# Kernel tuning notes

Hardware: AMD Instinct MI355X
Metric: run time of the kernel (lower is better)

Reference implementation:

```python
import jax, jax.numpy as jnp
import numpy as np

N = 100000   # n_node
D = 64       # emb_size
NNZ = 3200000
B, L = 64, 200
LAYERS = 2


def setup_inputs() -> dict:
    key = jax.random.key(0)
    ks = jax.random.split(key, 12)
    s = 1.0 / np.sqrt(D)  # reset_parameters uniform(-stdv, stdv)
    u = lambda k, shape: jax.random.uniform(k, shape, minval=-s, maxval=s, dtype=jnp.float32)
    return {
        "input": jax.random.randint(ks[0], (B, L), 0, N).astype(jnp.int32),
        "h_item_idx": jax.random.randint(ks[1], (2, NNZ), 0, N).astype(jnp.int32),
        "h_item_val": jax.random.uniform(ks[2], (NNZ,), dtype=jnp.float32),
        "h_user_idx": jax.random.randint(ks[3], (2, NNZ), 0, N).astype(jnp.int32),
        "h_user_val": jax.random.uniform(ks[4], (NNZ,), dtype=jnp.float32),
        "user_emb": u(ks[5], (N, D)),
        "w0": u(ks[6], (D, D)),
        "w1": u(ks[7], (D, D)),
        "b0": u(ks[8], (1, D)),
        "b1": u(ks[9], (1, D)),
        "att": u(ks[10], (1, D)),
        "att_m": u(ks[11], (D, D)),
    }


def _spmm(idx, val, x):
    # torch.sparse.mm(H, x) with H given as COO (rows=idx[0], cols=idx[1])
    gathered = val[:, None] * x[idx[1]]              # [nnz, D]
    return jax.ops.segment_sum(gathered, idx[0], num_segments=N)


def _l2norm(x):
    # F.normalize(x, p=2, dim=1), eps=1e-12
    n = jnp.maximum(jnp.linalg.norm(x, axis=1, keepdims=True), 1e-12)
    return x / n


def _structure_embed(h_item_idx, h_item_val, h_user_idx, h_user_val,
                     user_emb, w0, w1, b0, b1, att, att_m):
    # self_gating per channel (eval mode: no graph dropout)
    e2 = user_emb * jax.nn.sigmoid(user_emb @ w0 + b0)
    e3 = user_emb * jax.nn.sigmoid(user_emb @ w1 + b1)
    acc2, acc3 = e2, e3
    for _ in range(LAYERS):
        e2 = _spmm(h_item_idx, h_item_val, e2)
        acc2 = acc2 + _l2norm(e2)
        e3 = _spmm(h_user_idx, h_user_val, e3)
        acc3 = acc3 + _l2norm(e3)
    # channel attention over the two channel embeddings
    w_c2 = jnp.sum(att * (acc2 @ att_m), axis=1)     # [N]
    w_c3 = jnp.sum(att * (acc3 @ att_m), axis=1)     # [N]
    score = jax.nn.softmax(jnp.stack([w_c2, w_c3], axis=1), axis=-1)  # [N, 2]
    mixed = score[:, 0:1] * acc2 + score[:, 1:2] * acc3
    return mixed


def reference(input, h_item_idx, h_item_val, h_user_idx, h_user_val,
              user_emb, w0, w1, b0, b1, att, att_m):
    mask = input == 0                                 # [B, L]
    hg = _structure_embed(h_item_idx, h_item_val, h_user_idx, h_user_val,
                          user_emb, w0, w1, b0, b1, att, att_m)
    cas_seq_emb = hg[input]                           # [B, L, D]
    source_emb = cas_seq_emb[:, 0, :]                 # [B, D]
    # long-term attention: source query attends over the cascade sequence
    scores = jnp.einsum("bd,bld->bl", source_emb, cas_seq_emb) / np.sqrt(D)
    scores = jnp.where(mask, -1e9, scores)
    attw = jax.nn.softmax(scores, axis=-1)            # [B, L]
    L_cas_emb = attw[:, :, None] * cas_seq_emb        # [B, L, D]
    return (L_cas_emb, cas_seq_emb)
```

## Files before the change

### kernel.cpp

```cpp
#include <hip/hip_runtime.h>
#include <cstdint>
#include <cstddef>

#define N_NODES 100000
#define D 64
#define NNZ 3200000
#define BB 64
#define LL 200
#define BSHIFT 7
#define BSIZE 128
#define NBUCK 782
#define CAP 4608
#define EPT 9
#define BM_WORDS 3200

__device__ __forceinline__ float wave_sum(float x) {
#pragma unroll
  for (int o = 32; o; o >>= 1) x += __shfl_xor(x, o, 64);
  return x;
}

__global__ void mark_kernel(const int* __restrict__ input, uint32_t* __restrict__ bm,
                            int* __restrict__ list, int* __restrict__ nlist) {
  int t = blockIdx.x * 256 + threadIdx.x;
  if (t < BB * LL) {
    int i = input[t];
    uint32_t bit = 1u << (i & 31);
    uint32_t old = atomicOr(&bm[i >> 5], bit);
    if (!(old & bit)) {
      int p = atomicAdd(nlist, 1);
      list[p] = i;
    }
  }
}

__global__ __launch_bounds__(256) void gate_kernel(
    const float* __restrict__ u, const float* __restrict__ w0,
    const float* __restrict__ w1, const float* __restrict__ b0,
    const float* __restrict__ b1, float* __restrict__ e2, float* __restrict__ e3) {
  __shared__ float sw0[D * D];
  __shared__ float sw1[D * D];
  __shared__ float sb0[D], sb1[D];
  for (int t = threadIdx.x; t < D * D; t += 256) { sw0[t] = w0[t]; sw1[t] = w1[t]; }
  if (threadIdx.x < D) { sb0[threadIdx.x] = b0[threadIdx.x]; sb1[threadIdx.x] = b1[threadIdx.x]; }
  __syncthreads();
  int wave = (blockIdx.x * 256 + threadIdx.x) >> 6;
  int lane = threadIdx.x & 63;
  int nw = (gridDim.x * 256) >> 6;
  for (int i = wave; i < N_NODES; i += nw) {
    float uv = u[i * D + lane];
    float a0 = 0.f, a1 = 0.f;
#pragma unroll
    for (int k = 0; k < D; ++k) {
      float uk = __shfl(uv, k, 64);
      a0 = fmaf(uk, sw0[k * D + lane], a0);
      a1 = fmaf(uk, sw1[k * D + lane], a1);
    }
    a0 += sb0[lane];
    a1 += sb1[lane];
    float s0 = 1.f / (1.f + expf(-a0));
    float s1 = 1.f / (1.f + expf(-a1));
    e2[i * D + lane] = uv * s0;
    e3[i * D + lane] = uv * s1;
  }
}

__global__ void init_cursor_kernel(uint32_t* __restrict__ gcursor) {
  int t = blockIdx.x * 256 + threadIdx.x;
  if (t < NBUCK) gcursor[t] = (uint32_t)t * CAP;
}

__global__ __launch_bounds__(1024) void bin_kernel(
    const int* __restrict__ dsts, const int* __restrict__ srcs,
    const float* __restrict__ val, uint32_t* __restrict__ gcursor,
    uint2* __restrict__ binned) {
  __shared__ uint32_t hist[NBUCK];
  __shared__ uint32_t gbase[NBUCK];
  const int CHUNK = 8192;
  int base = blockIdx.x * CHUNK;
  int tid = threadIdx.x;
  for (int t = tid; t < NBUCK; t += 1024) hist[t] = 0u;
  __syncthreads();
  int n = NNZ - base;
  if (n > CHUNK) n = CHUNK;
  uint32_t px[8]; float pv[8]; uint32_t pb[8]; uint32_t pr[8];
#pragma unroll
  for (int k = 0; k < 8; ++k) {
    int off = (k << 10) + tid;
    bool ok = off < n;
    int e = base + off;
    int d = ok ? dsts[e] : 0;
    int s = ok ? srcs[e] : 0;
    float v = ok ? val[e] : 0.f;
    uint32_t b = (uint32_t)d >> BSHIFT;
    pb[k] = ok ? b : 0xFFFFFFFFu;
    pr[k] = ok ? atomicAdd(&hist[b], 1u) : 0u;
    px[k] = (uint32_t)s | ((uint32_t)(d & (BSIZE - 1)) << 17);
    pv[k] = v;
  }
  __syncthreads();
  for (int t = tid; t < NBUCK; t += 1024) {
    uint32_t h = hist[t];
    gbase[t] = h ? atomicAdd(&gcursor[t], h) : 0u;
  }
  __syncthreads();
#pragma unroll
  for (int k = 0; k < 8; ++k) {
    if (pb[k] != 0xFFFFFFFFu) {
      uint32_t pos = gbase[pb[k]] + pr[k];
      uint32_t lim = (pb[k] + 1u) * CAP;
      if (pos < lim) {
        binned[pos] = make_uint2(px[k], __float_as_uint(pv[k]));
      }
    }
  }
}

__global__ __launch_bounds__(512) void sortspmm_kernel(
    const uint32_t* __restrict__ gcursor, uint2* __restrict__ binned,
    const float* __restrict__ xin, float* __restrict__ xout,
    uint32_t* __restrict__ grow_start, uint32_t* __restrict__ grow_cnt) {
  __shared__ uint2 sp[CAP];
  __shared__ uint32_t hist[BSIZE];
  __shared__ uint32_t ssc[BSIZE];
  __shared__ uint32_t sst[BSIZE];
  int bucket = blockIdx.x, tid = threadIdx.x;
  int nodebase = bucket << BSHIFT;
  uint32_t cnt = gcursor[bucket] - (uint32_t)bucket * CAP;
  if (cnt > CAP) cnt = CAP;
  if (tid < BSIZE) hist[tid] = 0u;
  __syncthreads();
  uint2 pr[EPT]; uint32_t rk[EPT];
  const uint2* ep = binned + (size_t)bucket * CAP;
#pragma unroll
  for (int k = 0; k < EPT; ++k) {
    int e = (k << 9) + tid;
    if (e < (int)cnt) {
      pr[k] = ep[e];
      rk[k] = atomicAdd(&hist[pr[k].x >> 17], 1u);
    }
  }
  __syncthreads();
  if (tid < BSIZE) ssc[tid] = hist[tid];
  __syncthreads();
  for (int o = 1; o < BSIZE; o <<= 1) {
    uint32_t t = 0;
    if (tid < BSIZE && tid >= o) t = ssc[tid - o];
    __syncthreads();
    if (tid < BSIZE) ssc[tid] += t;
    __syncthreads();
  }
  if (tid < BSIZE) sst[tid] = ssc[tid] - hist[tid];
  __syncthreads();
#pragma unroll
  for (int k = 0; k < EPT; ++k) {
    int e = (k << 9) + tid;
    if (e < (int)cnt) sp[sst[pr[k].x >> 17] + rk[k]] = pr[k];
  }
  __syncthreads();
  for (int t = tid; t < (int)cnt; t += 512) binned[(size_t)bucket * CAP + t] = sp[t];
  int nvalid = N_NODES - nodebase;
  if (nvalid > BSIZE) nvalid = BSIZE;
  if (tid < nvalid) {
    grow_start[nodebase + tid] = (uint32_t)bucket * CAP + sst[tid];
    grow_cnt[nodebase + tid] = hist[tid];
  }
  int wave = tid >> 6, lane = tid & 63, g = lane >> 4, c = lane & 15;
  for (int r = wave; r < nvalid; r += 8) {
    uint32_t rc = hist[r], s0 = sst[r];
    float ax = 0.f, ay = 0.f, az = 0.f, aw = 0.f;
    uint32_t rc4 = (rc + 3u) & ~3u;
    for (uint32_t j = 0; j < rc4; j += 4) {
      uint32_t e = j + (uint32_t)g;
      uint2 p = make_uint2(0u, 0u);
      if (e < rc) p = sp[s0 + e];
      float v = __uint_as_float(p.y);
      uint32_t src = p.x & 0x1FFFFu;
      float4 xv = ((const float4*)(xin + (size_t)src * D))[c];
      ax = fmaf(v, xv.x, ax); ay = fmaf(v, xv.y, ay);
      az = fmaf(v, xv.z, az); aw = fmaf(v, xv.w, aw);
    }
#pragma unroll
    for (int o = 16; o <= 32; o <<= 1) {
      ax += __shfl_xor(ax, o, 64); ay += __shfl_xor(ay, o, 64);
      az += __shfl_xor(az, o, 64); aw += __shfl_xor(aw, o, 64);
    }
    if (g == 0)
      ((float4*)(xout + (size_t)(nodebase + r) * D))[c] = make_float4(ax, ay, az, aw);
  }
}

__global__ __launch_bounds__(256) void listspmm_kernel(
    const uint32_t* __restrict__ grow_start, const uint32_t* __restrict__ grow_cnt,
    const uint2* __restrict__ pairs, const float* __restrict__ xin,
    float* __restrict__ xout, const int* __restrict__ list, const int* __restrict__ nlist) {
  int wave = (blockIdx.x * 256 + threadIdx.x) >> 6;
  int lane = threadIdx.x & 63;
  int nw = (gridDim.x * 256) >> 6;
  int g = lane >> 4, c = lane & 15;
  int n = nlist[0];
  for (int ii = wave; ii < n; ii += nw) {
    int i = list[ii];
    uint32_t rc = grow_cnt[i];
    uint32_t base = grow_start[i];
    float ax = 0.f, ay = 0.f, az = 0.f, aw = 0.f;
    uint32_t rc4 = (rc + 3u) & ~3u;
    for (uint32_t j = 0; j < rc4; j += 4) {
      uint32_t e = j + (uint32_t)g;
      uint2 p = make_uint2(0u, 0u);
      if (e < rc) p = pairs[base + e];
      float v = __uint_as_float(p.y);
      uint32_t src = p.x & 0x1FFFFu;
      float4 xv = ((const float4*)(xin + (size_t)src * D))[c];
      ax = fmaf(v, xv.x, ax); ay = fmaf(v, xv.y, ay);
      az = fmaf(v, xv.z, az); aw = fmaf(v, xv.w, aw);
    }
#pragma unroll
    for (int o = 16; o <= 32; o <<= 1) {
      ax += __shfl_xor(ax, o, 64); ay += __shfl_xor(ay, o, 64);
      az += __shfl_xor(az, o, 64); aw += __shfl_xor(aw, o, 64);
    }
    if (g == 0)
      ((float4*)(xout + (size_t)i * D))[c] = make_float4(ax, ay, az, aw);
  }
}

__global__ __launch_bounds__(256) void final_kernel(
    const int* __restrict__ input,
    const float* __restrict__ e20, const float* __restrict__ e21, const float* __restrict__ e22,
    const float* __restrict__ e30, const float* __restrict__ e31, const float* __restrict__ e32,
    const float* __restrict__ att, const float* __restrict__ att_m,
    float* __restrict__ out_Lcas, float* __restrict__ out_cas) {
  __shared__ float cas[LL * D];
  __shared__ float sv[D];
  __shared__ float sscore[LL];
  __shared__ float red[8];
  int b = blockIdx.x, tid = threadIdx.x;
  if (tid < D) {
    float a = 0.f;
#pragma unroll
    for (int j = 0; j < D; ++j) a = fmaf(att_m[tid * D + j], att[j], a);
    sv[tid] = a;
  }
  __syncthreads();
  int wv = tid >> 6, lane = tid & 63;
  float svl = sv[lane];
  for (int l = wv; l < LL; l += 4) {
    int i = input[b * LL + l];
    size_t o = (size_t)i * D + lane;
    float v20 = e20[o], v21 = e21[o], v22 = e22[o];
    float v30 = e30[o], v31 = e31[o], v32 = e32[o];
    float n21 = fmaxf(sqrtf(wave_sum(v21 * v21)), 1e-12f);
    float n22 = fmaxf(sqrtf(wave_sum(v22 * v22)), 1e-12f);
    float n31 = fmaxf(sqrtf(wave_sum(v31 * v31)), 1e-12f);
    float n32 = fmaxf(sqrtf(wave_sum(v32 * v32)), 1e-12f);
    float a2 = v20 + v21 / n21 + v22 / n22;
    float a3 = v30 + v31 / n31 + v32 / n32;
    float w2 = wave_sum(a2 * svl);
    float w3 = wave_sum(a3 * svl);
    float mx = fmaxf(w2, w3);
    float ex2 = expf(w2 - mx), ex3 = expf(w3 - mx);
    float inv = 1.f / (ex2 + ex3);
    float mix = (ex2 * a2 + ex3 * a3) * inv;
    cas[l * D + lane] = mix;
    out_cas[(size_t)(b * LL + l) * D + lane] = mix;
  }
  __syncthreads();
  for (int l = wv; l < LL; l += 4) {
    float s = wave_sum(cas[lane] * cas[l * D + lane]) * 0.125f;
    int iv = input[b * LL + l];
    s = (iv == 0) ? -1e9f : s;
    if (lane == 0) sscore[l] = s;
  }
  __syncthreads();
  float m = -INFINITY;
  for (int l = tid; l < LL; l += 256) m = fmaxf(m, sscore[l]);
#pragma unroll
  for (int o = 32; o; o >>= 1) m = fmaxf(m, __shfl_xor(m, o, 64));
  if (lane == 0) red[wv] = m;
  __syncthreads();
  m = fmaxf(fmaxf(red[0], red[1]), fmaxf(red[2], red[3]));
  float sum = 0.f;
  for (int l = tid; l < LL; l += 256) sum += expf(sscore[l] - m);
  sum = wave_sum(sum);
  if (lane == 0) red[4 + wv] = sum;
  __syncthreads();
  float inv = 1.f / (red[4] + red[5] + red[6] + red[7]);
  for (int l = tid; l < LL; l += 256) sscore[l] = expf(sscore[l] - m) * inv;
  __syncthreads();
  for (int t = tid; t < LL * D; t += 256)
    out_Lcas[(size_t)b * LL * D + t] = sscore[t >> 6] * cas[t];
}

extern "C" void kernel_launch(void* const* d_in, const int* in_sizes, int n_in,
                              void* d_out, int out_size, void* d_ws, size_t ws_size,
                              hipStream_t stream) {
  const int* input = (const int*)d_in[0];
  const int* h_item_idx = (const int*)d_in[1];
  const float* h_item_val = (const float*)d_in[2];
  const int* h_user_idx = (const int*)d_in[3];
  const float* h_user_val = (const float*)d_in[4];
  const float* user_emb = (const float*)d_in[5];
  const float* w0 = (const float*)d_in[6];
  const float* w1 = (const float*)d_in[7];
  const float* b0 = (const float*)d_in[8];
  const float* b1 = (const float*)d_in[9];
  const float* att = (const float*)d_in[10];
  const float* att_m = (const float*)d_in[11];

  float* out = (float*)d_out;
  float* out_Lcas = out;
  float* out_cas = out + (size_t)BB * LL * D;

  const size_t ND = (size_t)N_NODES * D;
  char* ws = (char*)d_ws;
  float* e20 = (float*)ws; ws += ND * 4;
  float* e30 = (float*)ws; ws += ND * 4;
  float* e21 = (float*)ws; ws += ND * 4;
  float* e31 = (float*)ws; ws += ND * 4;
  float* e22 = (float*)ws; ws += ND * 4;
  float* e32 = (float*)ws; ws += ND * 4;
  uint2* binned = (uint2*)ws; ws += (size_t)NBUCK * CAP * 8;
  uint32_t* gcursor = (uint32_t*)ws; ws += (size_t)((NBUCK + 63) & ~63) * 4;
  uint32_t* bitmap = (uint32_t*)ws; ws += (size_t)BM_WORDS * 4;
  uint32_t* grow_start = (uint32_t*)ws; ws += (size_t)N_NODES * 4;
  uint32_t* grow_cnt = (uint32_t*)ws; ws += (size_t)N_NODES * 4;
  int* list = (int*)ws; ws += (size_t)(BB * LL) * 4;
  int* nlist = (int*)ws; ws += 64;

  const int* item_dst = h_item_idx;
  const int* item_src = h_item_idx + NNZ;
  const int* user_dst = h_user_idx;
  const int* user_src = h_user_idx + NNZ;

  const int BIN_BLOCKS = (NNZ + 8191) / 8192;

  hipMemsetAsync(bitmap, 0, (size_t)BM_WORDS * 4, stream);
  hipMemsetAsync(nlist, 0, 64, stream);
  mark_kernel<<<(BB * LL + 255) / 256, 256, 0, stream>>>(input, bitmap, list, nlist);

  gate_kernel<<<2048, 256, 0, stream>>>(user_emb, w0, w1, b0, b1, e20, e30);

  init_cursor_kernel<<<(NBUCK + 255) / 256, 256, 0, stream>>>(gcursor);
  bin_kernel<<<BIN_BLOCKS, 1024, 0, stream>>>(item_dst, item_src, h_item_val, gcursor, binned);
  sortspmm_kernel<<<NBUCK, 512, 0, stream>>>(gcursor, binned, e20, e21, grow_start, grow_cnt);
  listspmm_kernel<<<3200, 256, 0, stream>>>(grow_start, grow_cnt, binned, e21, e22, list, nlist);

  init_cursor_kernel<<<(NBUCK + 255) / 256, 256, 0, stream>>>(gcursor);
  bin_kernel<<<BIN_BLOCKS, 1024, 0, stream>>>(user_dst, user_src, h_user_val, gcursor, binned);
  sortspmm_kernel<<<NBUCK, 512, 0, stream>>>(gcursor, binned, e30, e31, grow_start, grow_cnt);
  listspmm_kernel<<<3200, 256, 0, stream>>>(grow_start, grow_cnt, binned, e31, e32, list, nlist);

  final_kernel<<<BB, 256, 0, stream>>>(input, e20, e21, e22, e30, e31, e32,
                                       att, att_m, out_Lcas, out_cas);
}
```

Measured before the change: 668.4 us.

## Stage binned edges in LDS for coalesced scatter; unroll SpMM gather loops by two

The bin kernel now locally sorts its chunk of edges by bucket in shared memory, using a prefix scan over bucket histograms. It then writes contiguous runs to the global bins, with a binary search mapping each slot to its bucket, instead of issuing scattered 8-byte writes. The chunk size is halved to fit the shared staging buffer, which doubles the block count and the global atomics on the bucket cursors. Separately, both SpMM gather loops process two edges per lane group per iteration to raise memory-level parallelism.

Measured after the change: 662.1 us. Within noise of the previous version (-1.0%).

```diff
diff --git a/kernel.cpp b/kernel.cpp
--- a/kernel.cpp
+++ b/kernel.cpp
@@ -13,6 +13,8 @@
 #define CAP 4608
 #define EPT 9
 #define BM_WORDS 3200
+#define BCHUNK 4096
+#define BEPT 4
 
 __device__ __forceinline__ float wave_sum(float x) {
 #pragma unroll
@@ -74,18 +76,19 @@
     const int* __restrict__ dsts, const int* __restrict__ srcs,
     const float* __restrict__ val, uint32_t* __restrict__ gcursor,
     uint2* __restrict__ binned) {
+  __shared__ uint2 sp[BCHUNK];
   __shared__ uint32_t hist[NBUCK];
+  __shared__ uint32_t sst[NBUCK + 1];
   __shared__ uint32_t gbase[NBUCK];
-  const int CHUNK = 8192;
-  int base = blockIdx.x * CHUNK;
+  int base = blockIdx.x * BCHUNK;
   int tid = threadIdx.x;
   for (int t = tid; t < NBUCK; t += 1024) hist[t] = 0u;
   __syncthreads();
   int n = NNZ - base;
-  if (n > CHUNK) n = CHUNK;
-  uint32_t px[8]; float pv[8]; uint32_t pb[8]; uint32_t pr[8];
-#pragma unroll
-  for (int k = 0; k < 8; ++k) {
+  if (n > BCHUNK) n = BCHUNK;
+  uint32_t px[BEPT]; float pv[BEPT]; uint32_t pb[BEPT]; uint32_t pr[BEPT];
+#pragma unroll
+  for (int k = 0; k < BEPT; ++k) {
     int off = (k << 10) + tid;
     bool ok = off < n;
     int e = base + off;
@@ -102,16 +105,32 @@
   for (int t = tid; t < NBUCK; t += 1024) {
     uint32_t h = hist[t];
     gbase[t] = h ? atomicAdd(&gcursor[t], h) : 0u;
-  }
-  __syncthreads();
-#pragma unroll
-  for (int k = 0; k < 8; ++k) {
-    if (pb[k] != 0xFFFFFFFFu) {
-      uint32_t pos = gbase[pb[k]] + pr[k];
-      uint32_t lim = (pb[k] + 1u) * CAP;
-      if (pos < lim) {
-        binned[pos] = make_uint2(px[k], __float_as_uint(pv[k]));
-      }
+    sst[t + 1] = h;
+  }
+  if (tid == 0) sst[0] = 0u;
+  __syncthreads();
+  for (int o = 1; o < NBUCK; o <<= 1) {
+    uint32_t t = 0u;
+    if (tid < NBUCK && (int)(tid + 1) > o) t = sst[tid + 1 - o];
+    __syncthreads();
+    if (tid < NBUCK && (int)(tid + 1) > o) sst[tid + 1] += t;
+    __syncthreads();
+  }
+#pragma unroll
+  for (int k = 0; k < BEPT; ++k) {
+    if (pb[k] != 0xFFFFFFFFu)
+      sp[sst[pb[k]] + pr[k]] = make_uint2(px[k], __float_as_uint(pv[k]));
+  }
+  __syncthreads();
+  for (int idx = tid; idx < n; idx += 1024) {
+    int lo = 0, hi = NBUCK;
+    while (hi - lo > 1) {
+      int mid = (lo + hi) >> 1;
+      if ((int)sst[mid] <= idx) lo = mid; else hi = mid;
+    }
+    uint32_t pos = gbase[lo] + ((uint32_t)idx - sst[lo]);
+    if (pos < (uint32_t)(lo + 1) * CAP) {
+      binned[pos] = sp[idx];
     }
   }
 }
@@ -169,16 +188,21 @@
   for (int r = wave; r < nvalid; r += 8) {
     uint32_t rc = hist[r], s0 = sst[r];
     float ax = 0.f, ay = 0.f, az = 0.f, aw = 0.f;
-    uint32_t rc4 = (rc + 3u) & ~3u;
-    for (uint32_t j = 0; j < rc4; j += 4) {
-      uint32_t e = j + (uint32_t)g;
-      uint2 p = make_uint2(0u, 0u);
-      if (e < rc) p = sp[s0 + e];
-      float v = __uint_as_float(p.y);
-      uint32_t src = p.x & 0x1FFFFu;
-      float4 xv = ((const float4*)(xin + (size_t)src * D))[c];
-      ax = fmaf(v, xv.x, ax); ay = fmaf(v, xv.y, ay);
-      az = fmaf(v, xv.z, az); aw = fmaf(v, xv.w, aw);
+    uint32_t rc8 = (rc + 7u) & ~7u;
+    for (uint32_t j = 0; j < rc8; j += 8) {
+      uint32_t e0 = j + (uint32_t)g;
+      uint32_t e1 = e0 + 4u;
+      uint2 p0 = make_uint2(0u, 0u), p1 = make_uint2(0u, 0u);
+      if (e0 < rc) p0 = sp[s0 + e0];
+      if (e1 < rc) p1 = sp[s0 + e1];
+      float v0 = __uint_as_float(p0.y), v1 = __uint_as_float(p1.y);
+      uint32_t sA = p0.x & 0x1FFFFu, sB = p1.x & 0x1FFFFu;
+      float4 x0 = ((const float4*)(xin + (size_t)sA * D))[c];
+      float4 x1 = ((const float4*)(xin + (size_t)sB * D))[c];
+      ax = fmaf(v0, x0.x, ax); ay = fmaf(v0, x0.y, ay);
+      az = fmaf(v0, x0.z, az); aw = fmaf(v0, x0.w, aw);
+      ax = fmaf(v1, x1.x, ax); ay = fmaf(v1, x1.y, ay);
+      az = fmaf(v1, x1.z, az); aw = fmaf(v1, x1.w, aw);
     }
 #pragma unroll
     for (int o = 16; o <= 32; o <<= 1) {
@@ -204,16 +228,21 @@
     uint32_t rc = grow_cnt[i];
     uint32_t base = grow_start[i];
     float ax = 0.f, ay = 0.f, az = 0.f, aw = 0.f;
-    uint32_t rc4 = (rc + 3u) & ~3u;
-    for (uint32_t j = 0; j < rc4; j += 4) {
-      uint32_t e = j + (uint32_t)g;
-      uint2 p = make_uint2(0u, 0u);
-      if (e < rc) p = pairs[base + e];
-      float v = __uint_as_float(p.y);
-      uint32_t src = p.x & 0x1FFFFu;
-      float4 xv = ((const float4*)(xin + (size_t)src * D))[c];
-      ax = fmaf(v, xv.x, ax); ay = fmaf(v, xv.y, ay);
-      az = fmaf(v, xv.z, az); aw = fmaf(v, xv.w, aw);
+    uint32_t rc8 = (rc + 7u) & ~7u;
+    for (uint32_t j = 0; j < rc8; j += 8) {
+      uint32_t e0 = j + (uint32_t)g;
+      uint32_t e1 = e0 + 4u;
+      uint2 p0 = make_uint2(0u, 0u), p1 = make_uint2(0u, 0u);
+      if (e0 < rc) p0 = pairs[base + e0];
+      if (e1 < rc) p1 = pairs[base + e1];
+      float v0 = __uint_as_float(p0.y), v1 = __uint_as_float(p1.y);
+      uint32_t sA = p0.x & 0x1FFFFu, sB = p1.x & 0x1FFFFu;
+      float4 x0 = ((const float4*)(xin + (size_t)sA * D))[c];
+      float4 x1 = ((const float4*)(xin + (size_t)sB * D))[c];
+      ax = fmaf(v0, x0.x, ax); ay = fmaf(v0, x0.y, ay);
+      az = fmaf(v0, x0.z, az); aw = fmaf(v0, x0.w, aw);
+      ax = fmaf(v1, x1.x, ax); ay = fmaf(v1, x1.y, ay);
+      az = fmaf(v1, x1.z, az); aw = fmaf(v1, x1.w, aw);
     }
 #pragma unroll
     for (int o = 16; o <= 32; o <<= 1) {
@@ -333,7 +362,7 @@
   const int* user_dst = h_user_idx;
   const int* user_src = h_user_idx + NNZ;
 
-  const int BIN_BLOCKS = (NNZ + 8191) / 8192;
+  const int BIN_BLOCKS = (NNZ + BCHUNK - 1) / BCHUNK;
 
   hipMemsetAsync(bitmap, 0, (size_t)BM_WORDS * 4, stream);
   hipMemsetAsync(nlist, 0, 64, stream);
```
